# Kernel optimization log

Hardware: AMD Instinct MI355X
Metric: run time of the kernel (lower is better)

## Reference

```python
import jax, jax.numpy as jnp
import numpy as np

B, T, C = 2, 2048, 2048
H, KVH, D = 16, 4, 128
EPS = 1.1920929e-07  # torch.finfo(float32).eps, default for F.rms_norm


def setup_inputs() -> dict:
    key = jax.random.key(0)
    ks = jax.random.split(key, 5)
    x = jax.random.normal(ks[0], (B, T, C), jnp.float32)
    # standard RoPE angle tables, shaped to broadcast over [B, T, heads, D/2]
    half = D // 2
    inv_freq = 1.0 / (10000.0 ** (np.arange(half, dtype=np.float64) / half))
    ang = np.arange(T, dtype=np.float64)[:, None] * inv_freq[None, :]
    cos = jnp.asarray(np.cos(ang), jnp.float32)[None, :, None, :]
    sin = jnp.asarray(np.sin(ang), jnp.float32)[None, :, None, :]
    s = C ** -0.5
    Wq = jax.random.normal(ks[1], (H * D, C), jnp.float32) * s
    Wk = jax.random.normal(ks[2], (KVH * D, C), jnp.float32) * s
    Wv = jax.random.normal(ks[3], (KVH * D, C), jnp.float32) * s
    Wo = jax.random.normal(ks[4], (C, C), jnp.float32) * s
    return {"x": x, "cos": cos, "sin": sin, "Wq": Wq, "Wk": Wk, "Wv": Wv, "Wo": Wo}


def _rope(x, cos, sin):
    d = x.shape[-1] // 2
    x1, x2 = x[..., :d], x[..., d:]
    return jnp.concatenate([x1 * cos + x2 * sin, -x1 * sin + x2 * cos], axis=-1)


def _rmsnorm(x):
    return x * jax.lax.rsqrt(jnp.mean(x * x, axis=-1, keepdims=True) + EPS)


def reference(x, cos, sin, Wq, Wk, Wv, Wo):
    Bx, Tx, Cx = x.shape
    q = (x @ Wq.T).reshape(Bx, Tx, H, D)
    k = (x @ Wk.T).reshape(Bx, Tx, KVH, D)
    v = (x @ Wv.T).reshape(Bx, Tx, KVH, D)
    q = _rmsnorm(_rope(q, cos, sin))
    k = _rmsnorm(_rope(k, cos, sin))
    # [B, heads, T, D]
    q = q.transpose(0, 2, 1, 3)
    k = k.transpose(0, 2, 1, 3)
    v = v.transpose(0, 2, 1, 3)
    groups = H // KVH  # GQA: replicate kv heads
    k = jnp.repeat(k, groups, axis=1)
    v = jnp.repeat(v, groups, axis=1)
    scale = 1.0 / jnp.sqrt(jnp.asarray(D, x.dtype))
    scores = jnp.einsum('bhqd,bhkd->bhqk', q, k) * scale
    causal = jnp.tril(jnp.ones((Tx, Tx), dtype=bool))
    scores = jnp.where(causal, scores, jnp.finfo(scores.dtype).min)
    att = jax.nn.softmax(scores, axis=-1)
    y = jnp.einsum('bhqk,bhkd->bhqd', att, v)
    y = y.transpose(0, 2, 1, 3).reshape(Bx, Tx, H * D)
    return y @ Wo.T
```

## Files before the change

### kernel.cpp

```cpp
#include <hip/hip_runtime.h>
#include <hip/hip_bf16.h>

typedef unsigned short u16t;
typedef unsigned int   u32t;
typedef float  f32x4 __attribute__((ext_vector_type(4)));
typedef short  s16x8 __attribute__((ext_vector_type(8)));
typedef unsigned int u32x4 __attribute__((ext_vector_type(4)));
typedef float  f4 __attribute__((ext_vector_type(4)));

#define BB 2
#define TT 2048
#define CC 2048
#define HH 16
#define KVHN 4
#define DD 128
#define EPSV 1.1920929e-07f
#define SCALE 0.08838834764831845f
#define MFIX 12.0f

__device__ __forceinline__ float b2f(u16t u){ union{u32t i; float f;} x; x.i=((u32t)u)<<16; return x.f; }
__device__ __forceinline__ u16t f2b(float f){ union{float f; u32t i;} x; x.f=f; u32t r = x.i + 0x7fffu + ((x.i>>16)&1u); return (u16t)(r>>16); }
__device__ __forceinline__ u32t pk2(float a, float b){
    __hip_bfloat162 h = __float22bfloat162_rn(make_float2(a,b));
    u32t r; __builtin_memcpy(&r,&h,4); return r;
}
__device__ __forceinline__ s16x8 ldf(const u16t* p){ s16x8 r; __builtin_memcpy(&r,p,16); return r; }
__device__ __forceinline__ void st16(u16t* p, u32x4 v){ __builtin_memcpy(p,&v,16); }
__device__ __forceinline__ u32x4 ldg16(const u16t* p){ u32x4 r; __builtin_memcpy(&r,p,16); return r; }

typedef const __attribute__((address_space(1))) unsigned int ga_u32;
typedef __attribute__((address_space(3))) unsigned int ls_u32;
__device__ __forceinline__ void gl16(const u16t* g, u16t* l) {
    __builtin_amdgcn_global_load_lds((ga_u32*)(unsigned long long)(g),
                                     (ls_u32*)(unsigned int)(unsigned long long)(l),
                                     16, 0, 0);
}

#define BARRIER() __builtin_amdgcn_s_barrier()
#define SCHEDB()  __builtin_amdgcn_sched_barrier(0)
#define WAITLG0() asm volatile("s_waitcnt lgkmcnt(0)" ::: "memory")
#define WAITLG4() asm volatile("s_waitcnt lgkmcnt(4)" ::: "memory")
#define WAITVM6() asm volatile("s_waitcnt vmcnt(6)" ::: "memory")
#define WAITVM5() asm volatile("s_waitcnt vmcnt(5)" ::: "memory")
#define WAITVM4() asm volatile("s_waitcnt vmcnt(4)" ::: "memory")
#define WAITVM0() asm volatile("s_waitcnt vmcnt(0)" ::: "memory")

__global__ __launch_bounds__(256) void cvt_kernel(
    const float* __restrict__ x,  const float* __restrict__ wq,
    const float* __restrict__ wk, const float* __restrict__ wv,
    const float* __restrict__ wo,
    u16t* __restrict__ xb, u16t* __restrict__ wqb, u16t* __restrict__ wkb,
    u16t* __restrict__ wvb, u16t* __restrict__ wob)
{
    size_t g = (size_t)blockIdx.x * 256 + threadIdx.x;
    const float* src; u16t* dst; size_t off;
    if      (g < 1048576) { src = x;  dst = xb;  off = g; }
    else if (g < 1572864) { src = wq; dst = wqb; off = g - 1048576; }
    else if (g < 1703936) { src = wk; dst = wkb; off = g - 1572864; }
    else if (g < 1835008) { src = wv; dst = wvb; off = g - 1703936; }
    else                  { src = wo; dst = wob; off = g - 1835008; }
    f4 a = *(const f4*)(src + off*8);
    f4 b = *(const f4*)(src + off*8 + 4);
    u32x4 o = { pk2(a[0],a[1]), pk2(a[2],a[3]), pk2(b[0],b[1]), pk2(b[2],b[3]) };
    st16(dst + off*8, o);
}

template<int NF, bool BSW>
__device__ __forceinline__ void gemm256(
    const u16t* __restrict__ aPanel, const u16t* __restrict__ bPanel,
    u16t* lds, f32x4 (&acc)[4][NF], const int tid)
{
    constexpr int BQ = NF/2;
    constexpr int BS = NF/4;
    u16t* Abuf[2] = { lds,         lds + 16384 };
    u16t* Bbuf[2] = { lds + 32768, lds + 32768 + NF*2048 };
    const int w = tid>>6, quad = (tid>>4)&3, l15 = tid&15;
    const int wr = (w>>1)*64, wc = (w&1)*(BQ*16);
    const int gcol = (((tid&7) ^ ((tid>>3)&7)) << 3);
    const u16t* aB  = aPanel + (size_t)(tid>>3)*CC + gcol;
    const u16t* bBr = bPanel + (size_t)(tid>>3)*CC + gcol;

    #pragma unroll
    for (int i=0;i<4;++i)
        #pragma unroll
        for (int j=0;j<NF;++j)
            #pragma unroll
            for (int r=0;r<4;++r) acc[i][j][r] = 0.f;

    #pragma unroll
    for (int i=0;i<4;++i) gl16(aB + (size_t)(i*64)*CC, Abuf[0] + (i*512+tid)*8);
    #pragma unroll
    for (int s=0;s<2*BS;++s){
        const int ss = BSW ? ((s==1)?2:((s==2)?1:s)) : s;
        gl16(bBr + (size_t)(ss*64)*CC, Bbuf[0] + (s*512+tid)*8);
    }
    SCHEDB();
    #pragma unroll
    for (int i=0;i<4;++i) gl16(aB + (size_t)(i*64)*CC + 64, Abuf[1] + (i*512+tid)*8);
    #pragma unroll
    for (int s=0;s<BS;++s){
        const int ss = BSW ? ((s==1)?2:s) : s;
        gl16(bBr + (size_t)(ss*64)*CC + 64, Bbuf[1] + (s*512+tid)*8);
    }

    s16x8 af0[4], af1[4], bf[BQ];

    #pragma unroll 2
    for (int kt=0; kt<32; ++kt){
        const u16t* Ac = Abuf[kt&1];
        const u16t* Bc = Bbuf[kt&1];
        u16t* An = Abuf[kt&1];
        u16t* Bn = Bbuf[kt&1];
        u16t* Bo = Bbuf[(kt+1)&1];
        if (kt == 31) { WAITVM0(); }
        else { if constexpr (NF==8) { WAITVM6(); } else { WAITVM5(); } }
        SCHEDB();
        BARRIER();

        #pragma unroll
        for (int mi=0;mi<4;++mi){
            const int row = wr + mi*16 + l15;
            af0[mi] = ldf(Ac + row*64 + ((quad ^ (row&7))<<3));
        }
        #pragma unroll
        for (int ni=0;ni<BQ;++ni){
            const int row = wc + ni*16 + l15;
            bf[ni] = ldf(Bc + row*64 + ((quad ^ (row&7))<<3));
        }
        #pragma unroll
        for (int mi=0;mi<4;++mi){
            const int row = wr + mi*16 + l15;
            af1[mi] = ldf(Ac + row*64 + (((4|quad) ^ (row&7))<<3));
        }
        SCHEDB();
        BARRIER();
        WAITLG4();
        SCHEDB();
        __builtin_amdgcn_s_setprio(1);
        #pragma unroll
        for (int mi=0;mi<4;++mi)
            #pragma unroll
            for (int ni=0;ni<BQ;++ni)
                acc[mi][ni] = __builtin_amdgcn_mfma_f32_16x16x32_bf16(
                    af0[mi], bf[ni], acc[mi][ni], 0,0,0);
        __builtin_amdgcn_s_setprio(0);

        #pragma unroll
        for (int ni=0;ni<BQ;++ni){
            const int row = wc + ni*16 + l15;
            bf[ni] = ldf(Bc + row*64 + (((4|quad) ^ (row&7))<<3));
        }
        if (kt < 31){
            #pragma unroll
            for (int s=0;s<BS;++s){
                const int sl = BS + s;
                const int ss = BSW ? ((sl==2)?1:sl) : sl;
                gl16(bBr + (size_t)(ss*64)*CC + (kt+1)*64, Bo + (sl*512+tid)*8);
            }
        }
        SCHEDB();
        BARRIER();
        WAITLG0();
        SCHEDB();
        __builtin_amdgcn_s_setprio(1);
        #pragma unroll
        for (int mi=0;mi<4;++mi)
            #pragma unroll
            for (int ni=0;ni<BQ;++ni)
                acc[mi][ni] = __builtin_amdgcn_mfma_f32_16x16x32_bf16(
                    af1[mi], bf[ni], acc[mi][ni], 0,0,0);
        __builtin_amdgcn_s_setprio(0);

        #pragma unroll
        for (int ni=0;ni<BQ;++ni){
            const int row = NF*16 + wc + ni*16 + l15;
            bf[ni] = ldf(Bc + row*64 + ((quad ^ (row&7))<<3));
        }
        if (kt < 30){
            #pragma unroll
            for (int i=0;i<4;++i)
                gl16(aB + (size_t)(i*64)*CC + (kt+2)*64, An + (i*512+tid)*8);
        }
        SCHEDB();
        BARRIER();
        WAITLG0();
        SCHEDB();
        __builtin_amdgcn_s_setprio(1);
        #pragma unroll
        for (int mi=0;mi<4;++mi)
            #pragma unroll
            for (int ni=0;ni<BQ;++ni)
                acc[mi][BQ+ni] = __builtin_amdgcn_mfma_f32_16x16x32_bf16(
                    af0[mi], bf[ni], acc[mi][BQ+ni], 0,0,0);
        __builtin_amdgcn_s_setprio(0);

        #pragma unroll
        for (int ni=0;ni<BQ;++ni){
            const int row = NF*16 + wc + ni*16 + l15;
            bf[ni] = ldf(Bc + row*64 + (((4|quad) ^ (row&7))<<3));
        }
        if (kt < 30){
            #pragma unroll
            for (int s=0;s<BS;++s){
                const int ss = BSW ? ((s==1)?2:s) : s;
                gl16(bBr + (size_t)(ss*64)*CC + (kt+2)*64, Bn + (s*512+tid)*8);
            }
        }
        SCHEDB();
        BARRIER();
        WAITLG0();
        SCHEDB();
        __builtin_amdgcn_s_setprio(1);
        #pragma unroll
        for (int mi=0;mi<4;++mi)
            #pragma unroll
            for (int ni=0;ni<BQ;++ni)
                acc[mi][BQ+ni] = __builtin_amdgcn_mfma_f32_16x16x32_bf16(
                    af1[mi], bf[ni], acc[mi][BQ+ni], 0,0,0);
        __builtin_amdgcn_s_setprio(0);
    }
}

__global__ __launch_bounds__(512,2) void qkv_kernel(
    const u16t* __restrict__ xb, const u16t* __restrict__ wqb,
    const u16t* __restrict__ wkb, const u16t* __restrict__ wvb,
    const float* __restrict__ cosp, const float* __restrict__ sinp,
    u16t* __restrict__ qws, u16t* __restrict__ kws, u16t* __restrict__ vtw)
{
    __shared__ __align__(16) u16t lds[65536];
    const int tid = threadIdx.x;
    const int bx = blockIdx.x, by = blockIdx.y;
    const int m0 = bx*256;

    int type, headbase; const u16t* W;
    if (by < 8)       { type=0; W = wqb + (size_t)by*256*CC;      headbase = by*2; }
    else if (by < 10) { type=1; W = wkb + (size_t)(by-8)*256*CC;  headbase = (by-8)*2; }
    else              { type=2; W = wvb + (size_t)(by-10)*256*CC; headbase = (by-10)*2; }

    f32x4 acc[4][8];
    gemm256<8,true>(xb + (size_t)m0*CC, W, lds, acc, tid);

    const int w = tid>>6, quad = (tid>>4)&3, l15 = tid&15;
    const int wr = (w>>1)*64, wn = w&1;
    const int head = headbase + wn;
    const int bb = bx>>3;
    const int ttb = (m0 + wr) & 2047;

    if (type == 2){
        u16t* vb = vtw + (size_t)(bb*KVHN+head)*DD*TT;
        #pragma unroll
        for (int mi=0;mi<4;++mi){
            const int tt = ttb + mi*16 + quad*4;
            #pragma unroll
            for (int ni=0;ni<8;++ni){
                const int d = ((ni>>2)*64) + ((ni&3)*16) + l15;
                u16t o[4];
                #pragma unroll
                for (int r=0;r<4;++r) o[r] = f2b(acc[mi][ni][r]);
                __builtin_memcpy(vb + (size_t)d*TT + tt, o, 8);
            }
        }
    } else {
        u16t* dst = (type==0) ? (qws + (size_t)(bb*HH+head)*TT*DD)
                              : (kws + (size_t)(bb*KVHN+head)*TT*DD);
        #pragma unroll
        for (int mi=0;mi<4;++mi){
            const int tt0 = ttb + mi*16 + quad*4;
            float ss[4] = {0.f,0.f,0.f,0.f};
            #pragma unroll
            for (int ni=0;ni<8;++ni)
                #pragma unroll
                for (int r=0;r<4;++r) ss[r] += acc[mi][ni][r]*acc[mi][ni][r];
            float rms[4];
            #pragma unroll
            for (int r=0;r<4;++r){
                float s = ss[r];
                s += __shfl_xor(s, 1, 16);
                s += __shfl_xor(s, 2, 16);
                s += __shfl_xor(s, 4, 16);
                s += __shfl_xor(s, 8, 16);
                rms[r] = rsqrtf(s*(1.f/128.f) + EPSV);
            }
            #pragma unroll
            for (int ni=0;ni<4;++ni){
                const int j = ni*16 + l15;
                #pragma unroll
                for (int r=0;r<4;++r){
                    const int tt = tt0 + r;
                    const float c = cosp[tt*64 + j];
                    const float s = sinp[tt*64 + j];
                    const float z1 = acc[mi][ni][r], z2 = acc[mi][ni+4][r];
                    dst[(size_t)tt*DD + j]      = f2b((z1*c + z2*s)*rms[r]);
                    dst[(size_t)tt*DD + j + 64] = f2b((z2*c - z1*s)*rms[r]);
                }
            }
        }
    }
}

__global__ __launch_bounds__(512,2) void attn_kernel(
    const u16t* __restrict__ qws, const u16t* __restrict__ kws,
    const u16t* __restrict__ vtw, u16t* __restrict__ yws)
{
    __shared__ __align__(16) u16t lds[49152];
    u16t* Ps = lds + 32768;

    const int tid = threadIdx.x;
    const int w = tid>>6, lane = tid&63, quad = lane>>4, l15 = lane&15;
    const int bx = blockIdx.x, h = blockIdx.y, b = blockIdx.z, kvh = h>>2;

    const int qti    = (w < 4) ? (15 - bx) : bx;
    const int qwbase = qti*128 + (w&3)*32;
    const int nkt    = (16 - bx)*2;

    const u16t* kb = kws + (size_t)(b*KVHN+kvh)*TT*DD;
    const u16t* vb = vtw + (size_t)(b*KVHN+kvh)*DD*TT;

    const int krow = tid>>4;
    const int kcg  = (tid&15) ^ ((tid>>4)&7);
    const int vrow = tid>>3;
    const int vcg  = (tid&7)  ^ ((tid>>3)&7);

    const u16t* qp = qws + ((size_t)(b*HH+h)*TT + qwbase + l15)*DD + quad*8;
    s16x8 qf[2][4];
    #pragma unroll
    for (int mi=0;mi<2;++mi)
        #pragma unroll
        for (int kq=0;kq<4;++kq)
            qf[mi][kq] = ldf(qp + (size_t)mi*16*DD + kq*32);

    {
        u16t* Kd = lds;        u16t* Vd = lds + 16384;
        gl16(kb + (size_t)(krow)*DD + kcg*8,        Kd + tid*8);
        gl16(kb + (size_t)(krow+32)*DD + kcg*8,     Kd + (512+tid)*8);
        gl16(vb + (size_t)(vrow)*TT + vcg*8,        Vd + tid*8);
        gl16(vb + (size_t)(vrow+64)*TT + vcg*8,     Vd + (512+tid)*8);
        SCHEDB();
        Kd = lds + 8192;       Vd = lds + 24576;
        gl16(kb + (size_t)(krow+64)*DD + kcg*8,      Kd + tid*8);
        gl16(kb + (size_t)(krow+96)*DD + kcg*8,      Kd + (512+tid)*8);
        gl16(vb + (size_t)(vrow)*TT + 64 + vcg*8,    Vd + tid*8);
        gl16(vb + (size_t)(vrow+64)*TT + 64 + vcg*8, Vd + (512+tid)*8);
    }

    f32x4 o_[2][8];
    float l_[2][4];
    #pragma unroll
    for (int mi=0;mi<2;++mi){
        #pragma unroll
        for (int r=0;r<4;++r) l_[mi][r] = 0.f;
        #pragma unroll
        for (int n8=0;n8<8;++n8)
            #pragma unroll
            for (int r=0;r<4;++r) o_[mi][n8][r] = 0.f;
    }

    const int swz = (l15&7)<<3;

    for (int kt=0; kt<nkt; ++kt){
        const int k0 = kt*64;
        if (kt+1 == nkt) { WAITVM0(); } else { WAITVM4(); }
        SCHEDB();
        BARRIER();
        if (k0 <= qwbase + 31) {
            const u16t* Ks = (kt&1) ? (lds + 8192)  : lds;
            const u16t* Vt = (kt&1) ? (lds + 24576) : (lds + 16384);

            f32x4 s[2][4];
            #pragma unroll
            for (int mi=0;mi<2;++mi)
                #pragma unroll
                for (int ni=0;ni<4;++ni)
                    #pragma unroll
                    for (int r=0;r<4;++r) s[mi][ni][r] = 0.f;
            #pragma unroll
            for (int kq=0;kq<4;++kq){
                s16x8 kf[4];
                #pragma unroll
                for (int ni=0;ni<4;++ni)
                    kf[ni] = ldf(Ks + (ni*16+l15)*128 + (((kq*4+quad)<<3) ^ swz));
                __builtin_amdgcn_s_setprio(1);
                #pragma unroll
                for (int mi=0;mi<2;++mi)
                    #pragma unroll
                    for (int ni=0;ni<4;++ni)
                        s[mi][ni] = __builtin_amdgcn_mfma_f32_16x16x32_bf16(qf[mi][kq], kf[ni], s[mi][ni], 0,0,0);
                __builtin_amdgcn_s_setprio(0);
            }

            const bool need_mask = (k0 + 63) > qwbase;
            #pragma unroll
            for (int mi=0;mi<2;++mi){
                const int qrow = qwbase + mi*16 + quad*4;
                #pragma unroll
                for (int ni=0;ni<4;++ni){
                    const int kcol = k0 + ni*16 + l15;
                    #pragma unroll
                    for (int r=0;r<4;++r){
                        float p = __expf(__builtin_fmaf(s[mi][ni][r], SCALE, -MFIX));
                        if (need_mask && kcol > qrow + r) p = 0.f;
                        l_[mi][r] += p;
                        const int rw = w*32 + mi*16 + quad*4 + r;
                        Ps[rw*64 + ((ni*16+l15) ^ (((quad*4+r)&7)<<3))] = f2b(p);
                    }
                }
            }

            #pragma unroll
            for (int ks=0;ks<2;++ks){
                s16x8 pf[2];
                #pragma unroll
                for (int mi=0;mi<2;++mi)
                    pf[mi] = ldf(Ps + (w*32+mi*16+l15)*64 + (((ks*4+quad)<<3) ^ swz));
                __builtin_amdgcn_s_setprio(1);
                #pragma unroll
                for (int n8=0;n8<8;++n8){
                    s16x8 vf = ldf(Vt + (n8*16+l15)*64 + (((ks*4+quad)<<3) ^ swz));
                    #pragma unroll
                    for (int mi=0;mi<2;++mi)
                        o_[mi][n8] = __builtin_amdgcn_mfma_f32_16x16x32_bf16(pf[mi], vf, o_[mi][n8], 0,0,0);
                }
                __builtin_amdgcn_s_setprio(0);
            }
        }
        BARRIER();
        if (kt+2 < nkt){
            const int kn = (kt+2)*64;
            u16t* Kd = (kt&1) ? (lds + 8192)  : lds;
            u16t* Vd = (kt&1) ? (lds + 24576) : (lds + 16384);
            gl16(kb + (size_t)(kn+krow)*DD + kcg*8,      Kd + tid*8);
            gl16(kb + (size_t)(kn+krow+32)*DD + kcg*8,   Kd + (512+tid)*8);
            gl16(vb + (size_t)(vrow)*TT + kn + vcg*8,    Vd + tid*8);
            gl16(vb + (size_t)(vrow+64)*TT + kn + vcg*8, Vd + (512+tid)*8);
        }
    }

    #pragma unroll
    for (int mi=0;mi<2;++mi){
        const int qrow = qwbase + mi*16 + quad*4;
        float inv[4];
        #pragma unroll
        for (int r=0;r<4;++r){
            float lt = l_[mi][r];
            lt += __shfl_xor(lt,1,16);
            lt += __shfl_xor(lt,2,16);
            lt += __shfl_xor(lt,4,16);
            lt += __shfl_xor(lt,8,16);
            inv[r] = 1.f/lt;
        }
        #pragma unroll
        for (int n8=0;n8<8;++n8)
            #pragma unroll
            for (int r=0;r<4;++r)
                yws[((size_t)(b*TT + qrow + r))*2048 + h*DD + n8*16 + l15] = f2b(o_[mi][n8][r]*inv[r]);
    }
}

__global__ __launch_bounds__(512,2) void oproj_kernel(
    const u16t* __restrict__ y, const u16t* __restrict__ wob, float* __restrict__ out)
{
    __shared__ __align__(16) u16t lds[49152];
    const int tid = threadIdx.x;
    const int m0 = blockIdx.x*256, n0 = blockIdx.y*128;

    f32x4 acc[4][4];
    gemm256<4,false>(y + (size_t)m0*CC, wob + (size_t)n0*CC, lds, acc, tid);

    const int w = tid>>6, quad = (tid>>4)&3, l15 = tid&15;
    const int wr = (w>>1)*64, wcq = (w&1)*32;
    #pragma unroll
    for (int mi=0;mi<4;++mi){
        const int m = m0 + wr + mi*16 + quad*4;
        #pragma unroll
        for (int ni=0;ni<4;++ni){
            const int n = n0 + ((ni>>1)*64) + wcq + ((ni&1)*16) + l15;
            #pragma unroll
            for (int r=0;r<4;++r)
                out[(size_t)(m+r)*CC + n] = acc[mi][ni][r];
        }
    }
}

extern "C" void kernel_launch(void* const* d_in, const int* in_sizes, int n_in,
                              void* d_out, int out_size, void* d_ws, size_t ws_size,
                              hipStream_t stream) {
    const float* x    = (const float*)d_in[0];
    const float* cosp = (const float*)d_in[1];
    const float* sinp = (const float*)d_in[2];
    const float* Wq   = (const float*)d_in[3];
    const float* Wk   = (const float*)d_in[4];
    const float* Wv   = (const float*)d_in[5];
    const float* Wo   = (const float*)d_in[6];

    u16t* ws  = (u16t*)d_ws;
    u16t* xb  = ws;
    u16t* wqb = xb  + 8388608;
    u16t* wkb = wqb + 4194304;
    u16t* wvb = wkb + 1048576;
    u16t* wob = wvb + 1048576;
    u16t* qws = wob + 4194304;
    u16t* kws = qws + 8388608;
    u16t* vtw = kws + 2097152;
    u16t* yws = xb;
    float* out = (float*)d_out;

    cvt_kernel<<<dim3(9216), 256, 0, stream>>>(x, Wq, Wk, Wv, Wo, xb, wqb, wkb, wvb, wob);
    qkv_kernel<<<dim3(16, 12), 512, 0, stream>>>(xb, wqb, wkb, wvb, cosp, sinp, qws, kws, vtw);
    attn_kernel<<<dim3(8, 16, 2), 512, 0, stream>>>(qws, kws, vtw, yws);
    oproj_kernel<<<dim3(16, 16), 512, 0, stream>>>(yws, wob, out);
}
```

Measured before the change: 302.6 us.

## Split attention blocks into 4-wave blocks of one query tile each

The attention kernel drops from 512-thread blocks, which paired a high and a low causal query tile, to 256-thread blocks that each handle a single 128-row query tile. The grid doubles to 16 tiles per head, and the batch index flips tile order to spread causal work. K/V staging loops are rewritten so 256 threads issue 4 loads each, with the vmcnt wait adjusted to match. LDS per block shrinks, which allows more blocks per CU, but each K/V tile is now loaded once per query tile instead of shared by two, so global traffic goes up and load balance relies on the scheduler.

After: 300.6 us. No clear change (-0.7%).

```diff
diff --git a/kernel.cpp b/kernel.cpp
--- a/kernel.cpp
+++ b/kernel.cpp
@@ -40,9 +40,9 @@
 #define SCHEDB()  __builtin_amdgcn_sched_barrier(0)
 #define WAITLG0() asm volatile("s_waitcnt lgkmcnt(0)" ::: "memory")
 #define WAITLG4() asm volatile("s_waitcnt lgkmcnt(4)" ::: "memory")
+#define WAITVM8() asm volatile("s_waitcnt vmcnt(8)" ::: "memory")
 #define WAITVM6() asm volatile("s_waitcnt vmcnt(6)" ::: "memory")
 #define WAITVM5() asm volatile("s_waitcnt vmcnt(5)" ::: "memory")
-#define WAITVM4() asm volatile("s_waitcnt vmcnt(4)" ::: "memory")
 #define WAITVM0() asm volatile("s_waitcnt vmcnt(0)" ::: "memory")
 
 __global__ __launch_bounds__(256) void cvt_kernel(
@@ -298,20 +298,20 @@
     }
 }
 
-__global__ __launch_bounds__(512,2) void attn_kernel(
+__global__ __launch_bounds__(256,2) void attn_kernel(
     const u16t* __restrict__ qws, const u16t* __restrict__ kws,
     const u16t* __restrict__ vtw, u16t* __restrict__ yws)
 {
-    __shared__ __align__(16) u16t lds[49152];
+    __shared__ __align__(16) u16t lds[40960];
     u16t* Ps = lds + 32768;
 
     const int tid = threadIdx.x;
     const int w = tid>>6, lane = tid&63, quad = lane>>4, l15 = lane&15;
     const int bx = blockIdx.x, h = blockIdx.y, b = blockIdx.z, kvh = h>>2;
 
-    const int qti    = (w < 4) ? (15 - bx) : bx;
-    const int qwbase = qti*128 + (w&3)*32;
-    const int nkt    = (16 - bx)*2;
+    const int qti    = b ? bx : (15 - bx);
+    const int qwbase = qti*128 + w*32;
+    const int nkt    = (qti+1)*2;
 
     const u16t* kb = kws + (size_t)(b*KVHN+kvh)*TT*DD;
     const u16t* vb = vtw + (size_t)(b*KVHN+kvh)*DD*TT;
@@ -328,19 +328,24 @@
         #pragma unroll
         for (int kq=0;kq<4;++kq)
             qf[mi][kq] = ldf(qp + (size_t)mi*16*DD + kq*32);
+    SCHEDB();
 
     {
         u16t* Kd = lds;        u16t* Vd = lds + 16384;
-        gl16(kb + (size_t)(krow)*DD + kcg*8,        Kd + tid*8);
-        gl16(kb + (size_t)(krow+32)*DD + kcg*8,     Kd + (512+tid)*8);
-        gl16(vb + (size_t)(vrow)*TT + vcg*8,        Vd + tid*8);
-        gl16(vb + (size_t)(vrow+64)*TT + vcg*8,     Vd + (512+tid)*8);
+        #pragma unroll
+        for (int j=0;j<4;++j)
+            gl16(kb + (size_t)(krow + j*16)*DD + kcg*8,      Kd + (j*256+tid)*8);
+        #pragma unroll
+        for (int j=0;j<4;++j)
+            gl16(vb + (size_t)(vrow + j*32)*TT + vcg*8,      Vd + (j*256+tid)*8);
         SCHEDB();
         Kd = lds + 8192;       Vd = lds + 24576;
-        gl16(kb + (size_t)(krow+64)*DD + kcg*8,      Kd + tid*8);
-        gl16(kb + (size_t)(krow+96)*DD + kcg*8,      Kd + (512+tid)*8);
-        gl16(vb + (size_t)(vrow)*TT + 64 + vcg*8,    Vd + tid*8);
-        gl16(vb + (size_t)(vrow+64)*TT + 64 + vcg*8, Vd + (512+tid)*8);
+        #pragma unroll
+        for (int j=0;j<4;++j)
+            gl16(kb + (size_t)(64 + krow + j*16)*DD + kcg*8, Kd + (j*256+tid)*8);
+        #pragma unroll
+        for (int j=0;j<4;++j)
+            gl16(vb + (size_t)(vrow + j*32)*TT + 64 + vcg*8, Vd + (j*256+tid)*8);
     }
 
     f32x4 o_[2][8];
@@ -359,7 +364,7 @@
 
     for (int kt=0; kt<nkt; ++kt){
         const int k0 = kt*64;
-        if (kt+1 == nkt) { WAITVM0(); } else { WAITVM4(); }
+        if (kt+1 == nkt) { WAITVM0(); } else { WAITVM8(); }
         SCHEDB();
         BARRIER();
         if (k0 <= qwbase + 31) {
@@ -428,10 +433,12 @@
             const int kn = (kt+2)*64;
             u16t* Kd = (kt&1) ? (lds + 8192)  : lds;
             u16t* Vd = (kt&1) ? (lds + 24576) : (lds + 16384);
-            gl16(kb + (size_t)(kn+krow)*DD + kcg*8,      Kd + tid*8);
-            gl16(kb + (size_t)(kn+krow+32)*DD + kcg*8,   Kd + (512+tid)*8);
-            gl16(vb + (size_t)(vrow)*TT + kn + vcg*8,    Vd + tid*8);
-            gl16(vb + (size_t)(vrow+64)*TT + kn + vcg*8, Vd + (512+tid)*8);
+            #pragma unroll
+            for (int j=0;j<4;++j)
+                gl16(kb + (size_t)(kn + krow + j*16)*DD + kcg*8, Kd + (j*256+tid)*8);
+            #pragma unroll
+            for (int j=0;j<4;++j)
+                gl16(vb + (size_t)(vrow + j*32)*TT + kn + vcg*8, Vd + (j*256+tid)*8);
         }
     }
 
@@ -506,6 +513,6 @@
 
     cvt_kernel<<<dim3(9216), 256, 0, stream>>>(x, Wq, Wk, Wv, Wo, xb, wqb, wkb, wvb, wob);
     qkv_kernel<<<dim3(16, 12), 512, 0, stream>>>(xb, wqb, wkb, wvb, cosp, sinp, qws, kws, vtw);
-    attn_kernel<<<dim3(8, 16, 2), 512, 0, stream>>>(qws, kws, vtw, yws);
+    attn_kernel<<<dim3(16, 16, 2), 256, 0, stream>>>(qws, kws, vtw, yws);
     oproj_kernel<<<dim3(16, 16), 512, 0, stream>>>(yws, wob, out);
 }
```
